# Optimization experiments

Measured on AMD Instinct MI355X. Metric: run time of the kernel, lower is better.

## Reference

```python
import jax, jax.numpy as jnp
import numpy as np

N_HEADS = 16


def setup_inputs() -> dict:
    key = jax.random.key(0)
    ks = jax.random.split(key, 8)
    ts, td, b, hc = 64, 4096, 8, 1024
    scale = 1.0 / np.sqrt(hc)
    return {
        "s": jax.random.normal(ks[0], (ts, b, hc), dtype=jnp.float32),
        "d": jax.random.normal(ks[1], (td, b, hc), dtype=jnp.float32),
        "Wq": jax.random.normal(ks[2], (hc, hc), dtype=jnp.float32) * scale,
        "bq": jax.random.normal(ks[3], (hc,), dtype=jnp.float32) * 0.01,
        "Wk": jax.random.normal(ks[4], (hc, hc), dtype=jnp.float32) * scale,
        "bk": jax.random.normal(ks[5], (hc,), dtype=jnp.float32) * 0.01,
        "Wv": jax.random.normal(ks[6], (hc, hc), dtype=jnp.float32) * scale,
        "bv": jax.random.normal(ks[7], (hc,), dtype=jnp.float32) * 0.01,
    }


def reference(s, d, Wq, bq, Wk, bk, Wv, bv):
    ts, b, hc = s.shape
    td = d.shape[0]
    h = N_HEADS
    c = hc // h
    # linear projections (torch Linear: x @ W.T + b)
    q = (s @ Wq.T + bq).reshape(ts, b, h, c)
    k = (d @ Wk.T + bk).reshape(td, b, h, c)
    v = (d @ Wv.T + bv).reshape(td, b, h, c)
    # scores over (slot, token) pairs, scaled
    a = jnp.einsum('sbhc,dbhc->sdbh', q, k) / jnp.sqrt(jnp.asarray(c, s.dtype))
    # competitive softmax across the SLOT axis (dim 0), not the key axis
    a = jax.nn.softmax(a, axis=0)          # (ts, td, b, h)
    n = jnp.sum(a, axis=1) + 0.001         # (ts, b, h)
    num = jnp.einsum('sdbh,dbhc->sbhc', a, v)
    out = num / n[..., None]               # normalized weighted average
    return out.reshape(ts, b, hc)
```

## Files before the change

kernel.cpp:

```cpp
#include <hip/hip_runtime.h>


#define TS 64
#define TD 4096
#define BATCH 8
#define HC 1024
#define NHEAD 16
#define MD (TD*BATCH)
#define MS (TS*BATCH)
#define NCHUNK 8
#define CHTOK (TD/NCHUNK)

typedef __attribute__((ext_vector_type(8))) __bf16 bf16x8;
typedef __attribute__((ext_vector_type(4))) float f32x4;
typedef __attribute__((ext_vector_type(4))) unsigned short u16x4;
typedef __attribute__((ext_vector_type(8))) unsigned short u16x8;

__device__ __forceinline__ unsigned short f2bf(float x){
  union { float f; unsigned u; } v; v.f = x;
  unsigned r = v.u + 0x7FFFu + ((v.u >> 16) & 1u);
  return (unsigned short)(r >> 16);
}

__device__ __forceinline__ void gll16(const void* g, void* l){
  __builtin_amdgcn_global_load_lds((__attribute__((address_space(1))) void*)g,
                                   (__attribute__((address_space(3))) void*)l, 16, 0, 0);
}

__global__ void cvt_bf16(const float* __restrict__ in, unsigned short* __restrict__ out, int n4){
  int i = blockIdx.x * blockDim.x + threadIdx.x;
  if (i >= n4) return;
  f32x4 f = ((const f32x4*)in)[i];
  u16x4 o;
  o[0] = f2bf(f[0]); o[1] = f2bf(f[1]); o[2] = f2bf(f[2]); o[3] = f2bf(f[3]);
  ((u16x4*)out)[i] = o;
}

__global__ __launch_bounds__(256) void gemm128(
    const unsigned short* __restrict__ A,
    const unsigned short* __restrict__ W,
    const float* __restrict__ bias,
    unsigned short* __restrict__ C)
{
  __shared__ unsigned short As[128*64];
  __shared__ unsigned short Bs[128*64];
  const int nwg = gridDim.x;
  const int cpx = nwg >> 3;
  const int orig = blockIdx.x;
  const int wg = (orig & 7) * cpx + (orig >> 3);
  const int mt = wg >> 3, nt = wg & 7;
  const int tid = threadIdx.x;
  const int lane = tid & 63, w = tid >> 6;
  const int l15 = lane & 15, lg = lane >> 4;
  const int wr = w >> 1, wc = w & 1;

  const int lrow = lane >> 3;
  const int lch  = (lane & 7) << 4;
  const char* pA[4]; const char* pB[4]; unsigned ldsoff[4];
  #pragma unroll
  for (int j = 0; j < 4; ++j){
    int row = w*32 + j*8 + lrow;
    int sw  = lch ^ ((row & 7) << 4);
    pA[j] = (const char*)A + (size_t)(mt*128 + row) * 2048 + sw;
    pB[j] = (const char*)W + (size_t)(nt*128 + row) * 2048 + sw;
    ldsoff[j] = (unsigned)(w*32 + j*8) * 128;
  }

  const f32x4 fz = {0.f, 0.f, 0.f, 0.f};
  f32x4 acc[4][4];
  #pragma unroll
  for (int m = 0; m < 4; ++m)
    #pragma unroll
    for (int n = 0; n < 4; ++n) acc[m][n] = fz;

  for (int kt = 0; kt < 16; ++kt){
    __syncthreads();
    #pragma unroll
    for (int j = 0; j < 4; ++j){
      gll16(pA[j] + (size_t)kt*128, (char*)As + ldsoff[j]);
      gll16(pB[j] + (size_t)kt*128, (char*)Bs + ldsoff[j]);
    }
    __syncthreads();
    #pragma unroll
    for (int kk = 0; kk < 2; ++kk){
      bf16x8 af[4], bfr[4];
      #pragma unroll
      for (int m = 0; m < 4; ++m){
        int row = wr*64 + m*16 + l15;
        af[m] = *(const bf16x8*)((const char*)As + row*128 + ((lg*16 + kk*64) ^ ((row & 7) << 4)));
      }
      #pragma unroll
      for (int n = 0; n < 4; ++n){
        int row = wc*64 + n*16 + l15;
        bfr[n] = *(const bf16x8*)((const char*)Bs + row*128 + ((lg*16 + kk*64) ^ ((row & 7) << 4)));
      }
      #pragma unroll
      for (int m = 0; m < 4; ++m)
        #pragma unroll
        for (int n = 0; n < 4; ++n)
          acc[m][n] = __builtin_amdgcn_mfma_f32_16x16x32_bf16(af[m], bfr[n], acc[m][n], 0, 0, 0);
    }
  }

  const int ccol0 = nt*128 + wc*64;
  float bv[4];
  #pragma unroll
  for (int n = 0; n < 4; ++n) bv[n] = bias[ccol0 + n*16 + l15];
  #pragma unroll
  for (int m = 0; m < 4; ++m){
    #pragma unroll
    for (int r = 0; r < 4; ++r){
      size_t row = (size_t)(mt*128 + wr*64 + m*16 + lg*4 + r);
      unsigned short* cp = C + row*1024 + ccol0;
      #pragma unroll
      for (int n = 0; n < 4; ++n)
        cp[n*16 + l15] = f2bf(acc[m][n][r] + bv[n]);
    }
  }
}

__global__ __launch_bounds__(256) void attn_kernel(
    const unsigned short* __restrict__ Q,
    const unsigned short* __restrict__ K,
    const unsigned short* __restrict__ V,
    float* __restrict__ P)
{
  __shared__ unsigned short Qs[64*64];
  __shared__ unsigned short Ks[64*64];
  __shared__ unsigned short Vt[80*64];
  __shared__ unsigned short Al[64*64];
  __shared__ float red[256];

  const int bh = blockIdx.x;
  const int chunk = blockIdx.y;
  const int bb = bh >> 4, h = bh & 15;
  const int tid = threadIdx.x;
  const int lane = tid & 63, w = tid >> 6;
  const int l15 = lane & 15, lg = lane >> 4;
  const int lrow = lane >> 3, lch = (lane & 7) << 4;

  for (int i = tid; i < 16*64; i += 256){
    int r = i >> 6;
    Vt[(64 + r)*64 + (i & 63)] = (r == 0) ? (unsigned short)0x3F80 : (unsigned short)0;
  }

  #pragma unroll
  for (int j = 0; j < 2; ++j){
    int row = w*16 + j*8 + lrow;
    int sw = lch ^ ((row & 7) << 4);
    const char* g = (const char*)Q + (size_t)(row*BATCH + bb)*2048 + h*128 + sw;
    gll16(g, (char*)Qs + (w*16 + j*8)*128);
  }

  const f32x4 fz = {0.f, 0.f, 0.f, 0.f};
  f32x4 acc[5];
  #pragma unroll
  for (int nb = 0; nb < 5; ++nb) acc[nb] = fz;

  const int vtok = tid >> 2;
  const int vcg  = tid & 3;
  const int t0 = chunk * CHTOK;

  for (int tt = 0; tt < CHTOK/64; ++tt){
    const int tb = t0 + tt*64;
    #pragma unroll
    for (int j = 0; j < 2; ++j){
      int row = w*16 + j*8 + lrow;
      int sw = lch ^ ((row & 7) << 4);
      const char* g = (const char*)K + (size_t)((size_t)(tb + row)*BATCH + bb)*2048 + h*128 + sw;
      gll16(g, (char*)Ks + (w*16 + j*8)*128);
    }
    const char* vg = (const char*)V + (size_t)((size_t)(tb + vtok)*BATCH + bb)*2048 + h*128 + vcg*32;
    u16x8 v0 = *(const u16x8*)vg;
    u16x8 v1 = *(const u16x8*)(vg + 16);
    __syncthreads();

    bf16x8 qa[2];
    #pragma unroll
    for (int kk = 0; kk < 2; ++kk){
      int row = w*16 + l15;
      qa[kk] = *(const bf16x8*)((const char*)Qs + row*128 + ((lg*16 + kk*64) ^ ((row & 7) << 4)));
    }
    float e[4][4];
    #pragma unroll
    for (int nb = 0; nb < 4; ++nb){
      f32x4 s = fz;
      #pragma unroll
      for (int kk = 0; kk < 2; ++kk){
        int row = nb*16 + l15;
        bf16x8 kb = *(const bf16x8*)((const char*)Ks + row*128 + ((lg*16 + kk*64) ^ ((row & 7) << 4)));
        s = __builtin_amdgcn_mfma_f32_16x16x32_bf16(qa[kk], kb, s, 0, 0, 0);
      }
      #pragma unroll
      for (int r = 0; r < 4; ++r) e[nb][r] = __expf(s[r] * 0.125f);
    }
    #pragma unroll
    for (int nb = 0; nb < 4; ++nb){
      float cp = e[nb][0] + e[nb][1] + e[nb][2] + e[nb][3];
      cp += __shfl_xor(cp, 16);
      cp += __shfl_xor(cp, 32);
      if (lg == 0) red[w*64 + nb*16 + l15] = cp;
    }
    __syncthreads();

    #pragma unroll
    for (int nb = 0; nb < 4; ++nb){
      int col = nb*16 + l15;
      float dn = red[col] + red[64 + col] + red[128 + col] + red[192 + col];
      float inv = 1.0f / dn;
      #pragma unroll
      for (int r = 0; r < 4; ++r){
        int row = w*16 + lg*4 + r;
        Al[row*64 + ((((2*col)) ^ ((row & 7) << 4)) >> 1)] = f2bf(e[nb][r] * inv);
      }
    }
    #pragma unroll
    for (int ee = 0; ee < 8; ++ee){
      int c0 = vcg*16 + ee;
      int sw0 = (((c0 & 7) ^ (c0 >> 3)) & 7) << 4;
      Vt[c0*64 + (((2*vtok) ^ sw0) >> 1)] = v0[ee];
    }
    #pragma unroll
    for (int ee = 0; ee < 8; ++ee){
      int c1 = vcg*16 + 8 + ee;
      int sw1 = (((c1 & 7) ^ (c1 >> 3)) & 7) << 4;
      Vt[c1*64 + (((2*vtok) ^ sw1) >> 1)] = v1[ee];
    }
    __syncthreads();

    bf16x8 aa[2];
    #pragma unroll
    for (int kk = 0; kk < 2; ++kk){
      int row = w*16 + l15;
      aa[kk] = *(const bf16x8*)((const char*)Al + row*128 + ((lg*16 + kk*64) ^ ((row & 7) << 4)));
    }
    #pragma unroll
    for (int nb = 0; nb < 5; ++nb){
      #pragma unroll
      for (int kk = 0; kk < 2; ++kk){
        int row = nb*16 + l15;
        int sw = (((row & 7) ^ (row >> 3)) & 7) << 4;
        bf16x8 vb = *(const bf16x8*)((const char*)Vt + row*128 + ((lg*16 + kk*64) ^ sw));
        acc[nb] = __builtin_amdgcn_mfma_f32_16x16x32_bf16(aa[kk], vb, acc[nb], 0, 0, 0);
      }
    }
  }

  float* Pb = P + (size_t)(bh*NCHUNK + chunk) * 64 * 80;
  #pragma unroll
  for (int nb = 0; nb < 5; ++nb){
    #pragma unroll
    for (int r = 0; r < 4; ++r){
      int s = w*16 + lg*4 + r;
      Pb[(size_t)s*80 + nb*16 + l15] = acc[nb][r];
    }
  }
}

__global__ void reduce_out(const float* __restrict__ P, float* __restrict__ out){
  int flat = blockIdx.x * 256 + threadIdx.x;
  int c = flat & 63, s = (flat >> 6) & 63, bh = flat >> 12;
  int bb = bh >> 4, h = bh & 15;
  float sc = 0.f, sn = 0.f;
  #pragma unroll
  for (int ch = 0; ch < NCHUNK; ++ch){
    const float* base = P + ((size_t)(bh*NCHUNK + ch)*64 + s)*80;
    sc += base[c];
    sn += base[64];
  }
  out[((size_t)s*BATCH + bb)*1024 + h*64 + c] = sc / (sn + 0.001f);
}

extern "C" void kernel_launch(void* const* d_in, const int* in_sizes, int n_in,
                              void* d_out, int out_size, void* d_ws, size_t ws_size,
                              hipStream_t stream)
{
  const float* s  = (const float*)d_in[0];
  const float* d  = (const float*)d_in[1];
  const float* Wq = (const float*)d_in[2];
  const float* bq = (const float*)d_in[3];
  const float* Wk = (const float*)d_in[4];
  const float* bk = (const float*)d_in[5];
  const float* Wv = (const float*)d_in[6];
  const float* bv = (const float*)d_in[7];
  float* out = (float*)d_out;

  char* ws = (char*)d_ws;
  unsigned short* dbf = (unsigned short*)(ws);
  unsigned short* sbf = (unsigned short*)(ws + 67108864);
  unsigned short* wqb = (unsigned short*)(ws + 68157440);
  unsigned short* wkb = (unsigned short*)(ws + 70254592);
  unsigned short* wvb = (unsigned short*)(ws + 72351744);
  unsigned short* Qw  = (unsigned short*)(ws + 74448896);
  unsigned short* Kw  = (unsigned short*)(ws + 75497472);
  unsigned short* Vw  = (unsigned short*)(ws + 142606336);
  float*          Pw  = (float*)(ws + 209715200);

  (void)in_sizes; (void)n_in; (void)out_size; (void)ws_size;

  cvt_bf16<<<(MD*HC/4 + 255)/256, 256, 0, stream>>>(d,  dbf, MD*HC/4);
  cvt_bf16<<<(MS*HC/4 + 255)/256, 256, 0, stream>>>(s,  sbf, MS*HC/4);
  cvt_bf16<<<(HC*HC/4 + 255)/256, 256, 0, stream>>>(Wq, wqb, HC*HC/4);
  cvt_bf16<<<(HC*HC/4 + 255)/256, 256, 0, stream>>>(Wk, wkb, HC*HC/4);
  cvt_bf16<<<(HC*HC/4 + 255)/256, 256, 0, stream>>>(Wv, wvb, HC*HC/4);

  gemm128<<<(MS/128)*8, 256, 0, stream>>>(sbf, wqb, bq, Qw);
  gemm128<<<(MD/128)*8, 256, 0, stream>>>(dbf, wkb, bk, Kw);
  gemm128<<<(MD/128)*8, 256, 0, stream>>>(dbf, wvb, bv, Vw);

  attn_kernel<<<dim3(128, NCHUNK), 256, 0, stream>>>(Qw, Kw, Vw, Pw);

  reduce_out<<<(TS*BATCH*HC)/256, 256, 0, stream>>>(Pw, out);
}
```

Before: 272.5 us.

## Fuse activation bf16 conversion into a single double-buffered QKV GEMM

The separate fp32-to-bf16 conversion passes over s and d are removed. The GEMM now streams fp32 activations into LDS and converts them to bf16 when loading fragments. The Q, K and V projections run in one launch with 256x128 tiles, using the contiguous Wk/Wv bf16 buffers as one 2048-row weight, plus LDS double buffering and MFMA priority hints. The three weight conversions are merged into one kernel. This is meant to cut the large extra read and write of d and several launches, at the cost of twice the LDS traffic for the fp32 A tiles and higher register pressure.

```diff
diff --git a/kernel.cpp b/kernel.cpp
--- a/kernel.cpp
+++ b/kernel.cpp
@@ -27,96 +27,149 @@
                                    (__attribute__((address_space(3))) void*)l, 16, 0, 0);
 }
 
-__global__ void cvt_bf16(const float* __restrict__ in, unsigned short* __restrict__ out, int n4){
-  int i = blockIdx.x * blockDim.x + threadIdx.x;
-  if (i >= n4) return;
-  f32x4 f = ((const f32x4*)in)[i];
+__global__ void cvt_w(const float* __restrict__ wq, const float* __restrict__ wk,
+                      const float* __restrict__ wv,
+                      unsigned short* __restrict__ wqb, unsigned short* __restrict__ wkb,
+                      unsigned short* __restrict__ wvb){
+  long i = (long)blockIdx.x * 256 + threadIdx.x;
+  const float* src; unsigned short* dst; long off;
+  if (i < 262144L)      { src = wq; dst = wqb; off = i; }
+  else if (i < 524288L) { src = wk; dst = wkb; off = i - 262144L; }
+  else                  { src = wv; dst = wvb; off = i - 524288L; }
+  f32x4 f = ((const f32x4*)src)[off];
   u16x4 o;
   o[0] = f2bf(f[0]); o[1] = f2bf(f[1]); o[2] = f2bf(f[2]); o[3] = f2bf(f[3]);
-  ((u16x4*)out)[i] = o;
-}
-
-__global__ __launch_bounds__(256) void gemm128(
-    const unsigned short* __restrict__ A,
-    const unsigned short* __restrict__ W,
-    const float* __restrict__ bias,
-    unsigned short* __restrict__ C)
+  ((u16x4*)dst)[off] = o;
+}
+
+__global__ __launch_bounds__(256, 2) void gemm_qkv(
+    const float* __restrict__ dA,
+    const float* __restrict__ sA,
+    const unsigned short* __restrict__ Wkv,
+    const unsigned short* __restrict__ Wq,
+    const float* __restrict__ bq,
+    const float* __restrict__ bk,
+    const float* __restrict__ bv,
+    unsigned short* __restrict__ Qout,
+    unsigned short* __restrict__ Kout,
+    unsigned short* __restrict__ Vout)
 {
-  __shared__ unsigned short As[128*64];
-  __shared__ unsigned short Bs[128*64];
+  __shared__ float          As[2][256*32];
+  __shared__ unsigned short Bs[2][128*32];
+
   const int nwg = gridDim.x;
   const int cpx = nwg >> 3;
   const int orig = blockIdx.x;
   const int wg = (orig & 7) * cpx + (orig >> 3);
-  const int mt = wg >> 3, nt = wg & 7;
   const int tid = threadIdx.x;
   const int lane = tid & 63, w = tid >> 6;
   const int l15 = lane & 15, lg = lane >> 4;
-  const int wr = w >> 1, wc = w & 1;
-
-  const int lrow = lane >> 3;
-  const int lch  = (lane & 7) << 4;
-  const char* pA[4]; const char* pB[4]; unsigned ldsoff[4];
-  #pragma unroll
-  for (int j = 0; j < 4; ++j){
-    int row = w*32 + j*8 + lrow;
-    int sw  = lch ^ ((row & 7) << 4);
-    pA[j] = (const char*)A + (size_t)(mt*128 + row) * 2048 + sw;
-    pB[j] = (const char*)W + (size_t)(nt*128 + row) * 2048 + sw;
-    ldsoff[j] = (unsigned)(w*32 + j*8) * 128;
-  }
+  const int wm = w >> 1, wn = w & 1;
+
+  const bool isQ = (wg >= 2048);
+  int mt, nt;
+  const float* Abase; const unsigned short* Wbase;
+  if (!isQ){ mt = wg >> 4; nt = wg & 15; Abase = dA; Wbase = Wkv; }
+  else     { int qi = wg - 2048; mt = qi >> 3; nt = qi & 7; Abase = sA; Wbase = Wq; }
+
+  const int a_r = lane >> 3;
+  const unsigned a_sw = (unsigned)(((lane & 7) ^ a_r) << 4);
+  const char* aS = (const char*)(Abase + (size_t)mt*256*1024) + a_sw;
+  unsigned a_src[8]; unsigned a_dst[8];
+  #pragma unroll
+  for (int j = 0; j < 8; ++j){
+    a_src[j] = (unsigned)((w*64 + j*8 + a_r) * 4096);
+    a_dst[j] = (unsigned)((w*64 + j*8) * 128);
+  }
+
+  const int b_r = lane >> 2;
+  const unsigned b_sw = (unsigned)(((lane & 3) ^ ((lane >> 3) & 3)) << 4);
+  const char* bS = (const char*)Wbase + (size_t)(nt*128) * 2048 + b_sw;
+  unsigned b_src[2]; unsigned b_dst[2];
+  #pragma unroll
+  for (int j = 0; j < 2; ++j){
+    b_src[j] = (unsigned)((j*64 + w*16 + b_r) * 2048);
+    b_dst[j] = (unsigned)((j*64 + w*16) * 64);
+  }
+
+  #define STAGE(t_, buf_) { \
+    const unsigned koA = (unsigned)(t_) * 128; \
+    const unsigned koB = (unsigned)(t_) * 64; \
+    char* dA_ = (char*)&As[buf_][0]; char* dB_ = (char*)&Bs[buf_][0]; \
+    _Pragma("unroll") \
+    for (int j = 0; j < 8; ++j) gll16(aS + a_src[j] + koA, dA_ + a_dst[j]); \
+    _Pragma("unroll") \
+    for (int j = 0; j < 2; ++j) gll16(bS + b_src[j] + koB, dB_ + b_dst[j]); \
+    __builtin_amdgcn_sched_barrier(0); }
+
+  const unsigned arow = (unsigned)(wm*128 + l15) * 128;
+  const unsigned ac0 = (unsigned)(((2*lg    ) ^ (l15 & 7)) << 4);
+  const unsigned ac1 = (unsigned)(((2*lg + 1) ^ (l15 & 7)) << 4);
+  const unsigned boff = (unsigned)(wn*64 + l15) * 64 + (unsigned)((lg ^ ((l15 >> 1) & 3)) << 4);
 
   const f32x4 fz = {0.f, 0.f, 0.f, 0.f};
-  f32x4 acc[4][4];
-  #pragma unroll
-  for (int m = 0; m < 4; ++m)
+  f32x4 acc[8][4];
+  #pragma unroll
+  for (int m = 0; m < 8; ++m)
     #pragma unroll
     for (int n = 0; n < 4; ++n) acc[m][n] = fz;
 
-  for (int kt = 0; kt < 16; ++kt){
-    __syncthreads();
-    #pragma unroll
-    for (int j = 0; j < 4; ++j){
-      gll16(pA[j] + (size_t)kt*128, (char*)As + ldsoff[j]);
-      gll16(pB[j] + (size_t)kt*128, (char*)Bs + ldsoff[j]);
-    }
-    __syncthreads();
-    #pragma unroll
-    for (int kk = 0; kk < 2; ++kk){
-      bf16x8 af[4], bfr[4];
-      #pragma unroll
-      for (int m = 0; m < 4; ++m){
-        int row = wr*64 + m*16 + l15;
-        af[m] = *(const bf16x8*)((const char*)As + row*128 + ((lg*16 + kk*64) ^ ((row & 7) << 4)));
-      }
-      #pragma unroll
-      for (int n = 0; n < 4; ++n){
-        int row = wc*64 + n*16 + l15;
-        bfr[n] = *(const bf16x8*)((const char*)Bs + row*128 + ((lg*16 + kk*64) ^ ((row & 7) << 4)));
-      }
-      #pragma unroll
-      for (int m = 0; m < 4; ++m)
-        #pragma unroll
-        for (int n = 0; n < 4; ++n)
-          acc[m][n] = __builtin_amdgcn_mfma_f32_16x16x32_bf16(af[m], bfr[n], acc[m][n], 0, 0, 0);
-    }
-  }
-
-  const int ccol0 = nt*128 + wc*64;
-  float bv[4];
-  #pragma unroll
-  for (int n = 0; n < 4; ++n) bv[n] = bias[ccol0 + n*16 + l15];
-  #pragma unroll
-  for (int m = 0; m < 4; ++m){
+  #define TILE(buf_) { \
+    const char* as_ = (const char*)&As[buf_][0]; \
+    const char* bs_ = (const char*)&Bs[buf_][0]; \
+    bf16x8 af[8]; bf16x8 bfr[4]; \
+    _Pragma("unroll") \
+    for (int m = 0; m < 8; ++m){ \
+      f32x4 u = *(const f32x4*)(as_ + arow + m*2048u + ac0); \
+      f32x4 v = *(const f32x4*)(as_ + arow + m*2048u + ac1); \
+      bf16x8 t; \
+      t[0] = (__bf16)u[0]; t[1] = (__bf16)u[1]; t[2] = (__bf16)u[2]; t[3] = (__bf16)u[3]; \
+      t[4] = (__bf16)v[0]; t[5] = (__bf16)v[1]; t[6] = (__bf16)v[2]; t[7] = (__bf16)v[3]; \
+      af[m] = t; \
+    } \
+    _Pragma("unroll") \
+    for (int n = 0; n < 4; ++n) bfr[n] = *(const bf16x8*)(bs_ + boff + n*1024u); \
+    __builtin_amdgcn_s_setprio(1); \
+    _Pragma("unroll") \
+    for (int m = 0; m < 8; ++m) \
+      _Pragma("unroll") \
+      for (int n = 0; n < 4; ++n) \
+        acc[m][n] = __builtin_amdgcn_mfma_f32_16x16x32_bf16(af[m], bfr[n], acc[m][n], 0, 0, 0); \
+    __builtin_amdgcn_s_setprio(0); }
+
+  STAGE(0, 0)
+  __syncthreads();
+
+  #pragma unroll 1
+  for (int tp = 0; tp < 16; ++tp){
+    STAGE(2*tp + 1, 1)
+    TILE(0)
+    __syncthreads();
+    if (tp < 15) STAGE(2*tp + 2, 0)
+    TILE(1)
+    __syncthreads();
+  }
+
+  int ccol; unsigned short* Cb; const float* bias;
+  if (isQ)          { Cb = Qout; bias = bq; ccol = nt*128 + wn*64; }
+  else if (nt < 8)  { Cb = Kout; bias = bk; ccol = nt*128 + wn*64; }
+  else              { Cb = Vout; bias = bv; ccol = (nt - 8)*128 + wn*64; }
+  float bvv[4];
+  #pragma unroll
+  for (int nf = 0; nf < 4; ++nf) bvv[nf] = bias[ccol + nf*16 + l15];
+  #pragma unroll
+  for (int mf = 0; mf < 8; ++mf){
     #pragma unroll
     for (int r = 0; r < 4; ++r){
-      size_t row = (size_t)(mt*128 + wr*64 + m*16 + lg*4 + r);
-      unsigned short* cp = C + row*1024 + ccol0;
-      #pragma unroll
-      for (int n = 0; n < 4; ++n)
-        cp[n*16 + l15] = f2bf(acc[m][n][r] + bv[n]);
-    }
-  }
+      size_t row = (size_t)(mt*256 + wm*128 + mf*16 + lg*4 + r);
+      __bf16* cp = (__bf16*)(Cb + row*1024 + ccol);
+      #pragma unroll
+      for (int nf = 0; nf < 4; ++nf)
+        cp[nf*16 + l15] = (__bf16)(acc[mf][nf][r] + bvv[nf]);
+    }
+  }
+  #undef STAGE
+  #undef TILE
 }
 
 __global__ __launch_bounds__(256) void attn_kernel(
@@ -286,8 +339,6 @@
   float* out = (float*)d_out;
 
   char* ws = (char*)d_ws;
-  unsigned short* dbf = (unsigned short*)(ws);
-  unsigned short* sbf = (unsigned short*)(ws + 67108864);
   unsigned short* wqb = (unsigned short*)(ws + 68157440);
   unsigned short* wkb = (unsigned short*)(ws + 70254592);
   unsigned short* wvb = (unsigned short*)(ws + 72351744);
@@ -298,15 +349,9 @@
 
   (void)in_sizes; (void)n_in; (void)out_size; (void)ws_size;
 
-  cvt_bf16<<<(MD*HC/4 + 255)/256, 256, 0, stream>>>(d,  dbf, MD*HC/4);
-  cvt_bf16<<<(MS*HC/4 + 255)/256, 256, 0, stream>>>(s,  sbf, MS*HC/4);
-  cvt_bf16<<<(HC*HC/4 + 255)/256, 256, 0, stream>>>(Wq, wqb, HC*HC/4);
-  cvt_bf16<<<(HC*HC/4 + 255)/256, 256, 0, stream>>>(Wk, wkb, HC*HC/4);
-  cvt_bf16<<<(HC*HC/4 + 255)/256, 256, 0, stream>>>(Wv, wvb, HC*HC/4);
-
-  gemm128<<<(MS/128)*8, 256, 0, stream>>>(sbf, wqb, bq, Qw);
-  gemm128<<<(MD/128)*8, 256, 0, stream>>>(dbf, wkb, bk, Kw);
-  gemm128<<<(MD/128)*8, 256, 0, stream>>>(dbf, wvb, bv, Vw);
+  cvt_w<<<3072, 256, 0, stream>>>(Wq, Wk, Wv, wqb, wkb, wvb);
+
+  gemm_qkv<<<2064, 256, 0, stream>>>(d, s, wkb, wqb, bq, bk, bv, Qw, Kw, Vw);
 
   attn_kernel<<<dim3(128, NCHUNK), 256, 0, stream>>>(Qw, Kw, Vw, Pw);
 
```

After: 308.0 us. 13.0% more time.
